# Kernel tuning notes

Hardware: AMD Instinct MI355X
Metric: run time of the kernel (lower is better)

## Reference

```python
import itertools
import jax, jax.numpy as jnp
import numpy as np


def setup_inputs() -> dict:
    key = jax.random.key(0)
    k1, k2 = jax.random.split(key)
    B, X, Y, Z, C = 2, 160, 192, 160, 1
    vol = jax.random.normal(k1, (B, X, Y, Z, C), dtype=jnp.float32)
    trf = jax.random.normal(k2, (B, X, Y, Z, 3), dtype=jnp.float32)  # dense displacement field
    return {"vol": vol, "trf": trf}


def _warp(vol, trf):
    # vol: [B, *spatial, C]; trf: [B, *spatial, nd] displacement (indexing='ij')
    B = vol.shape[0]
    spatial = vol.shape[1:-1]
    nd = len(spatial)
    C = vol.shape[-1]
    N = int(np.prod(spatial))

    grids = jnp.meshgrid(*[jnp.arange(s, dtype=jnp.float32) for s in spatial], indexing="ij")
    # absolute sample locations per dim: [B, *spatial]
    loc = [grids[d][None] + trf[..., d] for d in range(nd)]

    max_loc = [s - 1 for s in spatial]
    loc0 = [jnp.clip(jnp.floor(loc[d]), 0.0, max_loc[d]) for d in range(nd)]
    loc1 = [jnp.clip(loc0[d] + 1.0, 0.0, max_loc[d]) for d in range(nd)]
    clipped = [jnp.clip(loc[d], 0.0, max_loc[d]) for d in range(nd)]
    # neurite weight convention: weight for corner bit 0 is (loc1 - loc), for bit 1 is (1 - that)
    w1 = [loc1[d] - clipped[d] for d in range(nd)]   # weight when corner uses loc0
    w0 = [1.0 - w1[d] for d in range(nd)]            # weight when corner uses loc1
    i0 = [loc0[d].astype(jnp.int32) for d in range(nd)]
    i1 = [loc1[d].astype(jnp.int32) for d in range(nd)]

    vol_flat = vol.reshape(B, N, C)

    out = jnp.zeros((B,) + spatial + (C,), dtype=vol.dtype)
    for corner in itertools.product([0, 1], repeat=nd):
        subs = [(i1[d] if corner[d] else i0[d]) for d in range(nd)]
        ind = subs[0]
        for d in range(1, nd):
            ind = ind * spatial[d] + subs[d]  # row-major sub2ind
        vals = jnp.take_along_axis(vol_flat, ind.reshape(B, N)[..., None], axis=1)
        vals = vals.reshape((B,) + spatial + (C,))
        wt = (w0[0] if corner[0] else w1[0])
        for d in range(1, nd):
            wt = wt * (w0[d] if corner[d] else w1[d])
        out = out + wt[..., None] * vals
    return out


def reference(vol, trf):
    # indexing='ij', single_transform=False, fill_value=None (clamp to edge), linear interp.
    # The layer also passes trf through unchanged; we return the warped volume.
    return _warp(vol, trf)
```

## Files before the change

### kernel.cpp

```cpp
#include <hip/hip_runtime.h>

constexpr int B = 2, X = 160, Y = 192, Z = 160;
constexpr int TXs = 8, TYs = 8, TZs = 16;
constexpr int XT = X / TXs, YT = Y / TYs, ZT = Z / TZs;
constexpr int NTILES = B * XT * YT * ZT;
constexpr int NXCD = 8;
constexpr int CHUNK = NTILES / NXCD;
constexpr int RX = 15, RY = 16, RZ = 32;
constexpr int RSTRIDE = 33;
constexpr int NROWS = RX * RY;
constexpr int LDSF = NROWS * RSTRIDE;
constexpr int NCHUNKS = NROWS * 8;

typedef float f32x4 __attribute__((ext_vector_type(4)));
typedef float f32x2a __attribute__((ext_vector_type(2), aligned(4)));

__global__ __launch_bounds__(512, 8) void warp_kernel(
    const float* __restrict__ vol,
    const float* __restrict__ trf,
    float* __restrict__ out)
{
    __shared__ float lds[LDSF];

    const int tid = threadIdx.x;
    const int bid = blockIdx.x;

    const int eff = (bid & (NXCD - 1)) * CHUNK + (bid >> 3);

    int tz = eff % ZT;
    int r  = eff / ZT;
    int ty = r % YT;
    int r2 = r / YT;
    int tx = r2 % XT;
    int b  = r2 / XT;

    const int xs = tx * TXs - 4;
    const int ys = ty * TYs - 4;
    const int zs = tz * TZs - 8;
    const int bX = b * X;

    {
        int row = tid >> 3;
        int j   = tid & 7;
        bool interior = (xs >= 0) & (xs + RX <= X) &
                        (ys >= 0) & (ys + RY <= Y) &
                        (zs >= 0) & (zs + RZ <= Z);
        if (interior) {
            const float* gp = vol +
                ((size_t)(bX + xs + (row >> 4)) * Y + (ys + (row & 15))) * Z
                + (zs + 4 * j);
            int a = row * RSTRIDE + 4 * j;
#pragma unroll
            for (int k = 0; k < 4; ++k) {
                if (k < 3 || tid < NCHUNKS - 1536) {
                    f32x4 v = *reinterpret_cast<const f32x4*>(gp);
                    lds[a + 0] = v.x;
                    lds[a + 1] = v.y;
                    lds[a + 2] = v.z;
                    lds[a + 3] = v.w;
                }
                gp += (size_t)4 * Y * Z;
                a  += 64 * RSTRIDE;
            }
        } else {
#pragma unroll
            for (int k = 0; k < 4; ++k) {
                if (k < 3 || tid < NCHUNKS - 1536) {
                    int xi = row >> 4;
                    int yi = row & 15;
                    int xg = min(max(xs + xi, 0), X - 1);
                    int yg = min(max(ys + yi, 0), Y - 1);
                    int zg = min(max(zs + 4 * j, 0), Z - 4);
                    const f32x4 v = *reinterpret_cast<const f32x4*>(
                        vol + ((size_t)(bX + xg) * Y + yg) * Z + zg);
                    int a = row * RSTRIDE + 4 * j;
                    lds[a + 0] = v.x;
                    lds[a + 1] = v.y;
                    lds[a + 2] = v.z;
                    lds[a + 3] = v.w;
                }
                row += 64;
            }
        }
    }
    __syncthreads();

    int zq = tid & 7;
    int ly = (tid >> 3) & 7;
    int lx = tid >> 6;
    int x  = tx * TXs + lx;
    int y  = ty * TYs + ly;
    int z0v = tz * TZs + 2 * zq;

    size_t vid0 = ((size_t)(bX + x) * Y + y) * Z + z0v;

    const float* tb = trf + vid0 * 3;
    f32x4 ta = *reinterpret_cast<const f32x4*>(tb);
    f32x2a tc = *reinterpret_cast<const f32x2a*>(tb + 4);
    float d[6] = {ta.x, ta.y, ta.z, ta.w, tc.x, tc.y};

    const float c0x = (float)(-xs), c1x = (float)(X - 1 - xs);
    const float c0y = (float)(-ys), c1y = (float)(Y - 1 - ys);
    const float c0z = (float)(-zs), c1z = (float)(Z - 1 - zs);
    const float fxL = (float)(lx + 4);
    const float fyL = (float)(ly + 4);
    const float fzL = (float)(2 * zq + 8);

    float res[2];
#pragma unroll
    for (int e = 0; e < 2; ++e) {
        float rxf = __builtin_amdgcn_fmed3f(fxL + d[3 * e + 0], c0x, c1x);
        float ryf = __builtin_amdgcn_fmed3f(fyL + d[3 * e + 1], c0y, c1y);
        float rzf = __builtin_amdgcn_fmed3f((fzL + (float)e) + d[3 * e + 2], c0z, c1z);

        float flx = floorf(rxf), fly = floorf(ryf), flz = floorf(rzf);
        int ux0 = (int)flx, uy0 = (int)fly, uz0 = (int)flz;
        float fx = rxf - flx, fy = ryf - fly, fz = rzf - flz;

        bool ok = ((unsigned)ux0 < (unsigned)(RX - 1)) &
                  ((unsigned)uy0 < (unsigned)(RY - 1)) &
                  ((unsigned)uz0 < (unsigned)(RZ - 1));

        float v000, v001, v010, v011, v100, v101, v110, v111;
        if (ok) {
            int w = ((ux0 << 4) + uy0) * RSTRIDE + uz0;
            f32x2a p00 = *reinterpret_cast<const f32x2a*>(&lds[w]);
            f32x2a p01 = *reinterpret_cast<const f32x2a*>(&lds[w + RSTRIDE]);
            f32x2a p10 = *reinterpret_cast<const f32x2a*>(&lds[w + 16 * RSTRIDE]);
            f32x2a p11 = *reinterpret_cast<const f32x2a*>(&lds[w + 17 * RSTRIDE]);
            v000 = p00.x; v001 = p00.y;
            v010 = p01.x; v011 = p01.y;
            v100 = p10.x; v101 = p10.y;
            v110 = p11.x; v111 = p11.y;
        } else {
            int ix0 = ux0 + xs, iy0 = uy0 + ys, iz0 = uz0 + zs;
            ix0 = min(max(ix0, 0), X - 1);
            iy0 = min(max(iy0, 0), Y - 1);
            iz0 = min(max(iz0, 0), Z - 1);
            int ix1 = min(ix0 + 1, X - 1);
            int iy1 = min(iy0 + 1, Y - 1);
            int iz1 = min(iz0 + 1, Z - 1);
            size_t g00 = ((size_t)(bX + ix0) * Y + iy0) * Z;
            size_t g01 = ((size_t)(bX + ix0) * Y + iy1) * Z;
            size_t g10 = ((size_t)(bX + ix1) * Y + iy0) * Z;
            size_t g11 = ((size_t)(bX + ix1) * Y + iy1) * Z;
            v000 = vol[g00 + iz0];
            v001 = vol[g00 + iz1];
            v010 = vol[g01 + iz0];
            v011 = vol[g01 + iz1];
            v100 = vol[g10 + iz0];
            v101 = vol[g10 + iz1];
            v110 = vol[g11 + iz0];
            v111 = vol[g11 + iz1];
        }

        float c00 = v000 + fz * (v001 - v000);
        float c01 = v010 + fz * (v011 - v010);
        float c10 = v100 + fz * (v101 - v100);
        float c11 = v110 + fz * (v111 - v110);
        float c0  = c00 + fy * (c01 - c00);
        float c1  = c10 + fy * (c11 - c10);
        res[e] = c0 + fx * (c1 - c0);
    }

    f32x2a o;
    o.x = res[0]; o.y = res[1];
    *reinterpret_cast<f32x2a*>(out + vid0) = o;
}

extern "C" void kernel_launch(void* const* d_in, const int* in_sizes, int n_in,
                              void* d_out, int out_size, void* d_ws, size_t ws_size,
                              hipStream_t stream) {
    const float* vol = (const float*)d_in[0];
    const float* trf = (const float*)d_in[1];
    float* out = (float*)d_out;

    warp_kernel<<<NTILES, 512, 0, stream>>>(vol, trf, out);
}
```

Measured before the change: 40.96 us.

## Enlarge warp tiles to 16x16x16 with 1024 threads and 4 voxels per thread

Tiles grow from 8x8x16 to 16x16x16 voxels, so the LDS halo region becomes 23x24x32 and each block gets 1024 threads that each produce 4 consecutive z outputs. The aim is to cut the halo overhead per output, cut the number of blocks, and widen the trf and out accesses to full 16-byte vectors. The LDS fill now does vectorised 16-byte stores on interior tiles, and the LDS buffer moves to dynamic shared memory of about 73KB. The cost is much larger LDS per block and higher register pressure, which limits occupancy to roughly one or two blocks per CU. It also calls hipFuncSetAttribute on every launch.

```diff
diff --git a/kernel.cpp b/kernel.cpp
--- a/kernel.cpp
+++ b/kernel.cpp
@@ -1,26 +1,27 @@
 #include <hip/hip_runtime.h>
 
 constexpr int B = 2, X = 160, Y = 192, Z = 160;
-constexpr int TXs = 8, TYs = 8, TZs = 16;
+constexpr int TXs = 16, TYs = 16, TZs = 16;
 constexpr int XT = X / TXs, YT = Y / TYs, ZT = Z / TZs;
 constexpr int NTILES = B * XT * YT * ZT;
 constexpr int NXCD = 8;
 constexpr int CHUNK = NTILES / NXCD;
-constexpr int RX = 15, RY = 16, RZ = 32;
+constexpr int RX = 23, RY = 24, RZ = 32;
 constexpr int RSTRIDE = 33;
 constexpr int NROWS = RX * RY;
 constexpr int LDSF = NROWS * RSTRIDE;
+constexpr int LDSB = LDSF * 4;
 constexpr int NCHUNKS = NROWS * 8;
 
 typedef float f32x4 __attribute__((ext_vector_type(4)));
 typedef float f32x2a __attribute__((ext_vector_type(2), aligned(4)));
 
-__global__ __launch_bounds__(512, 8) void warp_kernel(
+__global__ __launch_bounds__(1024, 8) void warp_kernel(
     const float* __restrict__ vol,
     const float* __restrict__ trf,
     float* __restrict__ out)
 {
-    __shared__ float lds[LDSF];
+    extern __shared__ float lds[];
 
     const int tid = threadIdx.x;
     const int bid = blockIdx.x;
@@ -40,75 +41,79 @@
     const int bX = b * X;
 
     {
-        int row = tid >> 3;
-        int j   = tid & 7;
+        int row0 = tid >> 3;
+        int j    = tid & 7;
         bool interior = (xs >= 0) & (xs + RX <= X) &
                         (ys >= 0) & (ys + RY <= Y) &
                         (zs >= 0) & (zs + RZ <= Z);
         if (interior) {
+            unsigned ux = (unsigned)row0 / 24u;
+            int      uy = row0 - 24 * (int)ux;
             const float* gp = vol +
-                ((size_t)(bX + xs + (row >> 4)) * Y + (ys + (row & 15))) * Z
-                + (zs + 4 * j);
-            int a = row * RSTRIDE + 4 * j;
+                ((size_t)(bX + xs + (int)ux) * Y + (ys + uy)) * Z + (zs + 4 * j);
+            int a = row0 * RSTRIDE + 4 * j;
 #pragma unroll
-            for (int k = 0; k < 4; ++k) {
-                if (k < 3 || tid < NCHUNKS - 1536) {
+            for (int k = 0; k < 5; ++k) {
+                if (k < 4 || tid < NCHUNKS - 4096) {
                     f32x4 v = *reinterpret_cast<const f32x4*>(gp);
+                    *reinterpret_cast<f32x4*>(&lds[a]) = v;
+                }
+                int uyn = uy + 8;
+                bool wrap = (uyn >= 24);
+                gp += wrap ? (size_t)(6 * Y - 16) * Z : (size_t)(5 * Y + 8) * Z;
+                uy  = wrap ? uyn - 24 : uyn;
+                a  += 128 * RSTRIDE;
+            }
+        } else {
+#pragma unroll
+            for (int k = 0; k < 5; ++k) {
+                int c = tid + k * 1024;
+                if (c < NCHUNKS) {
+                    int row = c >> 3;
+                    int jj  = c & 7;
+                    unsigned ux = (unsigned)row / 24u;
+                    int      uy = row - 24 * (int)ux;
+                    int xg = min(max(xs + (int)ux, 0), X - 1);
+                    int yg = min(max(ys + uy, 0), Y - 1);
+                    int zg = min(max(zs + 4 * jj, 0), Z - 4);
+                    const f32x4 v = *reinterpret_cast<const f32x4*>(
+                        vol + ((size_t)(bX + xg) * Y + yg) * Z + zg);
+                    int a = row * RSTRIDE + 4 * jj;
                     lds[a + 0] = v.x;
                     lds[a + 1] = v.y;
                     lds[a + 2] = v.z;
                     lds[a + 3] = v.w;
                 }
-                gp += (size_t)4 * Y * Z;
-                a  += 64 * RSTRIDE;
-            }
-        } else {
-#pragma unroll
-            for (int k = 0; k < 4; ++k) {
-                if (k < 3 || tid < NCHUNKS - 1536) {
-                    int xi = row >> 4;
-                    int yi = row & 15;
-                    int xg = min(max(xs + xi, 0), X - 1);
-                    int yg = min(max(ys + yi, 0), Y - 1);
-                    int zg = min(max(zs + 4 * j, 0), Z - 4);
-                    const f32x4 v = *reinterpret_cast<const f32x4*>(
-                        vol + ((size_t)(bX + xg) * Y + yg) * Z + zg);
-                    int a = row * RSTRIDE + 4 * j;
-                    lds[a + 0] = v.x;
-                    lds[a + 1] = v.y;
-                    lds[a + 2] = v.z;
-                    lds[a + 3] = v.w;
-                }
-                row += 64;
             }
         }
     }
     __syncthreads();
 
-    int zq = tid & 7;
-    int ly = (tid >> 3) & 7;
+    int zq = tid & 3;
+    int ly = (tid >> 2) & 15;
     int lx = tid >> 6;
     int x  = tx * TXs + lx;
     int y  = ty * TYs + ly;
-    int z0v = tz * TZs + 2 * zq;
+    int z0v = tz * TZs + 4 * zq;
 
     size_t vid0 = ((size_t)(bX + x) * Y + y) * Z + z0v;
 
-    const float* tb = trf + vid0 * 3;
-    f32x4 ta = *reinterpret_cast<const f32x4*>(tb);
-    f32x2a tc = *reinterpret_cast<const f32x2a*>(tb + 4);
-    float d[6] = {ta.x, ta.y, ta.z, ta.w, tc.x, tc.y};
+    const f32x4* tp = reinterpret_cast<const f32x4*>(trf + vid0 * 3);
+    f32x4 t0 = tp[0], t1 = tp[1], t2 = tp[2];
+    float d[12] = {t0.x, t0.y, t0.z, t0.w,
+                   t1.x, t1.y, t1.z, t1.w,
+                   t2.x, t2.y, t2.z, t2.w};
 
     const float c0x = (float)(-xs), c1x = (float)(X - 1 - xs);
     const float c0y = (float)(-ys), c1y = (float)(Y - 1 - ys);
     const float c0z = (float)(-zs), c1z = (float)(Z - 1 - zs);
     const float fxL = (float)(lx + 4);
     const float fyL = (float)(ly + 4);
-    const float fzL = (float)(2 * zq + 8);
+    const float fzL = (float)(4 * zq + 8);
 
-    float res[2];
+    float res[4];
 #pragma unroll
-    for (int e = 0; e < 2; ++e) {
+    for (int e = 0; e < 4; ++e) {
         float rxf = __builtin_amdgcn_fmed3f(fxL + d[3 * e + 0], c0x, c1x);
         float ryf = __builtin_amdgcn_fmed3f(fyL + d[3 * e + 1], c0y, c1y);
         float rzf = __builtin_amdgcn_fmed3f((fzL + (float)e) + d[3 * e + 2], c0z, c1z);
@@ -123,11 +128,11 @@
 
         float v000, v001, v010, v011, v100, v101, v110, v111;
         if (ok) {
-            int w = ((ux0 << 4) + uy0) * RSTRIDE + uz0;
+            int w = (ux0 * 24 + uy0) * RSTRIDE + uz0;
             f32x2a p00 = *reinterpret_cast<const f32x2a*>(&lds[w]);
             f32x2a p01 = *reinterpret_cast<const f32x2a*>(&lds[w + RSTRIDE]);
-            f32x2a p10 = *reinterpret_cast<const f32x2a*>(&lds[w + 16 * RSTRIDE]);
-            f32x2a p11 = *reinterpret_cast<const f32x2a*>(&lds[w + 17 * RSTRIDE]);
+            f32x2a p10 = *reinterpret_cast<const f32x2a*>(&lds[w + 24 * RSTRIDE]);
+            f32x2a p11 = *reinterpret_cast<const f32x2a*>(&lds[w + 25 * RSTRIDE]);
             v000 = p00.x; v001 = p00.y;
             v010 = p01.x; v011 = p01.y;
             v100 = p10.x; v101 = p10.y;
@@ -163,9 +168,9 @@
         res[e] = c0 + fx * (c1 - c0);
     }
 
-    f32x2a o;
-    o.x = res[0]; o.y = res[1];
-    *reinterpret_cast<f32x2a*>(out + vid0) = o;
+    f32x4 o;
+    o.x = res[0]; o.y = res[1]; o.z = res[2]; o.w = res[3];
+    *reinterpret_cast<f32x4*>(out + vid0) = o;
 }
 
 extern "C" void kernel_launch(void* const* d_in, const int* in_sizes, int n_in,
@@ -175,5 +180,8 @@
     const float* trf = (const float*)d_in[1];
     float* out = (float*)d_out;
 
-    warp_kernel<<<NTILES, 512, 0, stream>>>(vol, trf, out);
+    hipFuncSetAttribute(reinterpret_cast<const void*>(warp_kernel),
+                        hipFuncAttributeMaxDynamicSharedMemorySize, LDSB);
+
+    warp_kernel<<<NTILES, 1024, LDSB, stream>>>(vol, trf, out);
 }
```

New measurement: 52.25 us. +27.6%, slower.
